# Performance work log

Measured on AMD Instinct MI355X. Metric: run time of the kernel, lower is better.

## Reference

```python
import jax, jax.numpy as jnp
import numpy as np

B, S, H, DH = 2, 2048, 24, 32
E = H * DH  # 768


def setup_inputs() -> dict:
    key = jax.random.key(0)
    ks = jax.random.split(key, 7)
    embedding = jax.random.normal(ks[0], (B, S, E), dtype=jnp.float32)
    mask = jax.random.randint(ks[1], (B, S, S), 0, 2).astype(bool)
    # per-head QKV weights (applied as x @ W, equivalent param to torch Linear W.T)
    Wq = jax.random.normal(ks[2], (H, DH, DH), dtype=jnp.float32) * 0.05
    Wk = jax.random.normal(ks[3], (H, DH, DH), dtype=jnp.float32) * 0.05
    Wv = jax.random.normal(ks[4], (H, DH, DH), dtype=jnp.float32) * 0.05
    Wo = jax.random.normal(ks[5], (E, E), dtype=jnp.float32) * 0.02
    bo = jax.random.normal(ks[6], (E,), dtype=jnp.float32) * 0.02
    return {"embedding": embedding, "mask": mask, "Wq": Wq, "Wk": Wk,
            "Wv": Wv, "Wo": Wo, "bo": bo}


def reference(embedding, mask, Wq, Wk, Wv, Wo, bo):
    # split channels into heads: [B,S,H,DH]
    xh = embedding.reshape(B, S, H, DH)
    # per-head projections (batched over heads)
    Q = jnp.einsum('bshd,hde->bhse', xh, Wq)
    K = jnp.einsum('bshd,hde->bhse', xh, Wk)
    V = jnp.einsum('bshd,hde->bhse', xh, Wv)
    scale = 1.0 / jnp.sqrt(jnp.float32(DH))
    scores = jnp.einsum('bhqd,bhkd->bhqk', Q, K) * scale
    # faithful quirk: masked positions set to -1e-6 (not -inf)
    scores = jnp.where(mask[:, None, :, :], scores, jnp.float32(-1e-6))
    probs = jax.nn.softmax(scores, axis=-1)
    out = jnp.einsum('bhqk,bhkd->bqhd', probs, V)  # [B,S,H,DH]
    out = out.reshape(B, S, E)  # concat heads along feature dim
    return out @ Wo.T + bo
```

## Files before the change

### kernel.cpp

```cpp
#include <hip/hip_runtime.h>
#include <hip/hip_bf16.h>

#define B_  2
#define S_  2048
#define H_  24
#define DH_ 32
#define E_  768
#define SW_ (S_/32)

#define NB_MASK ((B_*S_*S_)/256)
#define NB_WO   ((E_*E_)/1024)
#define NB_WT   (H_)

typedef __attribute__((ext_vector_type(8))) short short8;
typedef __attribute__((ext_vector_type(4))) float f32x4;

static __device__ __forceinline__ float bf16tof(short s) {
    unsigned u = ((unsigned)(unsigned short)s) << 16;
    return __builtin_bit_cast(float, u);
}
static __device__ __forceinline__ short4 pack4(float a, float b, float c, float d) {
    union { __hip_bfloat162 h[2]; short4 s; } u;
    u.h[0] = __float22bfloat162_rn(make_float2(a, b));
    u.h[1] = __float22bfloat162_rn(make_float2(c, d));
    return u.s;
}
static __device__ __forceinline__ short8 pack8f(const float* a, const float* b) {
    union { __hip_bfloat162 h[4]; short8 s; } u;
    u.h[0] = __float22bfloat162_rn(make_float2(a[0], a[1]));
    u.h[1] = __float22bfloat162_rn(make_float2(a[2], a[3]));
    u.h[2] = __float22bfloat162_rn(make_float2(b[0], b[1]));
    u.h[3] = __float22bfloat162_rn(make_float2(b[2], b[3]));
    return u.s;
}
static __device__ __forceinline__ short8 pack8(float4 a, float4 b) {
    union { __hip_bfloat162 h[4]; short8 s; } u;
    u.h[0] = __float22bfloat162_rn(make_float2(a.x, a.y));
    u.h[1] = __float22bfloat162_rn(make_float2(a.z, a.w));
    u.h[2] = __float22bfloat162_rn(make_float2(b.x, b.y));
    u.h[3] = __float22bfloat162_rn(make_float2(b.z, b.w));
    return u.s;
}

#define QSCALE  0.25503487f
#define MEXP    0.99999899864f

__global__ __launch_bounds__(256) void prep_kernel(
    const int* __restrict__ mask, const float* __restrict__ Wo,
    const float* __restrict__ Wq, const float* __restrict__ Wk,
    const float* __restrict__ Wv,
    unsigned int* __restrict__ mbits, __hip_bfloat16* __restrict__ Wob,
    __hip_bfloat16* __restrict__ WTq, __hip_bfloat16* __restrict__ WTk,
    __hip_bfloat16* __restrict__ WTv)
{
    const int bx = blockIdx.x;
    if (bx < NB_MASK) {
        const int idx  = bx * 256 + threadIdx.x;
        const int lane = threadIdx.x & 63;
        const unsigned long long bal = __ballot(mask[idx] != 0);
        if (lane == 0) {
            uint2 w;
            w.x = (unsigned int)(bal & 0xffffffffull);
            w.y = (unsigned int)(bal >> 32);
            *reinterpret_cast<uint2*>(mbits + (idx >> 5)) = w;
        }
    } else if (bx < NB_MASK + NB_WO) {
        const int i = ((bx - NB_MASK) * 256 + threadIdx.x) * 4;
        const float4 w = *reinterpret_cast<const float4*>(Wo + i);
        *reinterpret_cast<short4*>(Wob + i) = pack4(w.x, w.y, w.z, w.w);
    } else {
        const int h = bx - NB_MASK - NB_WO;
        const int base = h * DH_ * DH_;
        for (int i = threadIdx.x; i < DH_ * DH_; i += 256) {
            const int d = i >> 5, e = i & 31;
            WTq[base + e * 32 + d] = __float2bfloat16(Wq[base + i]);
            WTk[base + e * 32 + d] = __float2bfloat16(Wk[base + i]);
            WTv[base + e * 32 + d] = __float2bfloat16(Wv[base + i]);
        }
    }
}

__global__ __launch_bounds__(256) void qkv_kernel(
    const float* __restrict__ x,
    const __hip_bfloat16* __restrict__ WTq,
    const __hip_bfloat16* __restrict__ WTk,
    const __hip_bfloat16* __restrict__ WTv,
    __hip_bfloat16* __restrict__ Qo,
    __hip_bfloat16* __restrict__ Ko,
    __hip_bfloat16* __restrict__ Vto)
{
    const int bh   = blockIdx.y;
    const int b    = bh / H_;
    const int h    = bh - b * H_;
    const int wave = threadIdx.x >> 6;
    const int lane = threadIdx.x & 63;
    const int col  = lane & 15;
    const int quad = lane >> 4;
    const int sw   = blockIdx.x * 64 + wave * 16;
    const int s    = sw + col;

    const float* xp = x + ((size_t)b * S_ + s) * E_ + h * DH_ + quad * 8;
    const float4 xa = *reinterpret_cast<const float4*>(xp);
    const float4 xb = *reinterpret_cast<const float4*>(xp + 4);
    const short8 xf = pack8(xa, xb);

    const int wofs = h * DH_ * DH_ + col * 32 + quad * 8;
    const short8 aQ0 = *reinterpret_cast<const short8*>(WTq + wofs);
    const short8 aQ1 = *reinterpret_cast<const short8*>(WTq + wofs + 16 * 32);
    const short8 aK0 = *reinterpret_cast<const short8*>(WTk + wofs);
    const short8 aK1 = *reinterpret_cast<const short8*>(WTk + wofs + 16 * 32);
    const short8 bV0 = *reinterpret_cast<const short8*>(WTv + wofs);
    const short8 bV1 = *reinterpret_cast<const short8*>(WTv + wofs + 16 * 32);

    const f32x4 z = {0.f, 0.f, 0.f, 0.f};
    const f32x4 qt0 = __builtin_amdgcn_mfma_f32_16x16x32_bf16(aQ0, xf, z, 0, 0, 0);
    const f32x4 qt1 = __builtin_amdgcn_mfma_f32_16x16x32_bf16(aQ1, xf, z, 0, 0, 0);
    const f32x4 kt0 = __builtin_amdgcn_mfma_f32_16x16x32_bf16(aK0, xf, z, 0, 0, 0);
    const f32x4 kt1 = __builtin_amdgcn_mfma_f32_16x16x32_bf16(aK1, xf, z, 0, 0, 0);
    const f32x4 vv0 = __builtin_amdgcn_mfma_f32_16x16x32_bf16(xf, bV0, z, 0, 0, 0);
    const f32x4 vv1 = __builtin_amdgcn_mfma_f32_16x16x32_bf16(xf, bV1, z, 0, 0, 0);

    __hip_bfloat16* qrow = Qo + ((size_t)bh * S_ + s) * DH_;
    *reinterpret_cast<short4*>(qrow + quad * 4) =
        pack4(qt0[0] * QSCALE, qt0[1] * QSCALE, qt0[2] * QSCALE, qt0[3] * QSCALE);
    *reinterpret_cast<short4*>(qrow + 16 + quad * 4) =
        pack4(qt1[0] * QSCALE, qt1[1] * QSCALE, qt1[2] * QSCALE, qt1[3] * QSCALE);

    const int t32  = s & 31;
    const int slot = (s & ~31) | (((t32 >> 2) & 1) << 4)
                   | (((t32 >> 3) << 2) | (t32 & 3));
    __hip_bfloat16* krow = Ko + ((size_t)bh * S_ + slot) * DH_;
    *reinterpret_cast<short4*>(krow + quad * 4)      = pack4(kt0[0], kt0[1], kt0[2], kt0[3]);
    *reinterpret_cast<short4*>(krow + 16 + quad * 4) = pack4(kt1[0], kt1[1], kt1[2], kt1[3]);

    const int sb = sw + quad * 4;
    *reinterpret_cast<short4*>(Vto + ((size_t)bh * DH_ + col) * S_ + sb) =
        pack4(vv0[0], vv0[1], vv0[2], vv0[3]);
    *reinterpret_cast<short4*>(Vto + ((size_t)bh * DH_ + 16 + col) * S_ + sb) =
        pack4(vv1[0], vv1[1], vv1[2], vv1[3]);
}

__global__ __launch_bounds__(256) void attn_kernel(
    const __hip_bfloat16* __restrict__ Q,
    const __hip_bfloat16* __restrict__ K,
    const __hip_bfloat16* __restrict__ Vt,
    const unsigned int* __restrict__ mbits,
    __hip_bfloat16* __restrict__ Opart,
    float* __restrict__ lpart,
    int parts)
{
    const int bid  = blockIdx.x;
    const int xcd  = bid & 7;
    const int t_   = bid >> 3;
    const int bh   = xcd * 6 + (t_ % 6);
    const int rest = t_ / 6;
    const int qblk = rest & 7;
    const int part = rest >> 3;

    const int b    = bh / H_;
    const int h    = bh - b * H_;
    const int niter = S_ / (64 * parts);
    const int kbeg  = part * (S_ / parts);
    const int wave = threadIdx.x >> 6;
    const int lane = threadIdx.x & 63;
    const int col  = lane & 15;
    const int quad = lane >> 4;
    const int q0   = qblk * 256 + wave * 64;

    const __hip_bfloat16* Qbh = Q  + (size_t)bh * S_ * DH_;
    const __hip_bfloat16* Kbh = K  + (size_t)bh * S_ * DH_;
    const __hip_bfloat16* Vbh = Vt + (size_t)bh * DH_ * S_;

    short8 qf[4];
#pragma unroll
    for (int t = 0; t < 4; ++t)
        qf[t] = *reinterpret_cast<const short8*>(
            Qbh + (size_t)(q0 + t * 16 + col) * DH_ + quad * 8);

    const __hip_bfloat16* Kp  = Kbh + (size_t)(kbeg + col) * DH_ + quad * 8;
    const __hip_bfloat16* Vp0 = Vbh + (size_t)col * S_ + kbeg + quad * 8;
    const __hip_bfloat16* Vp1 = Vbh + (size_t)(16 + col) * S_ + kbeg + quad * 8;
    const unsigned int* mbb = mbits + (size_t)b * S_ * SW_ + (kbeg >> 5);
    const unsigned int* mp[4];
#pragma unroll
    for (int t = 0; t < 4; ++t)
        mp[t] = mbb + (size_t)(q0 + t * 16 + col) * SW_;

    const short ONE = 0x3F80;
    const short8 ones = {ONE, ONE, ONE, ONE, ONE, ONE, ONE, ONE};

    f32x4 o0a[4], o1a[4], la[4];
#pragma unroll
    for (int t = 0; t < 4; ++t) {
        o0a[t] = (f32x4){0.f,0.f,0.f,0.f};
        o1a[t] = (f32x4){0.f,0.f,0.f,0.f};
        la[t]  = (f32x4){0.f,0.f,0.f,0.f};
    }

    for (int it = 0; it < niter; ++it) {
        uint2 mw[4];
#pragma unroll
        for (int t = 0; t < 4; ++t)
            mw[t] = *reinterpret_cast<const uint2*>(mp[t]);

        const short8 kA0 = *reinterpret_cast<const short8*>(Kp);
        const short8 kA1 = *reinterpret_cast<const short8*>(Kp + 16 * DH_);
        const short8 vA0 = *reinterpret_cast<const short8*>(Vp0);
        const short8 vA1 = *reinterpret_cast<const short8*>(Vp1);
        const short8 kB0 = *reinterpret_cast<const short8*>(Kp + 32 * DH_);
        const short8 kB1 = *reinterpret_cast<const short8*>(Kp + 48 * DH_);
        const short8 vB0 = *reinterpret_cast<const short8*>(Vp0 + 32);
        const short8 vB1 = *reinterpret_cast<const short8*>(Vp1 + 32);

        const f32x4 z = {0.f, 0.f, 0.f, 0.f};

        f32x4 s0[4], s1[4];
#pragma unroll
        for (int t = 0; t < 4; ++t) {
            s0[t] = __builtin_amdgcn_mfma_f32_16x16x32_bf16(kA0, qf[t], z, 0, 0, 0);
            s1[t] = __builtin_amdgcn_mfma_f32_16x16x32_bf16(kA1, qf[t], z, 0, 0, 0);
        }
#pragma unroll
        for (int t = 0; t < 4; ++t) {
            float p0[4], p1[4];
#pragma unroll
            for (int r = 0; r < 4; ++r) {
                const int kb = quad * 8 + r;
                const float e0 = __builtin_amdgcn_exp2f(s0[t][r]);
                const float e1 = __builtin_amdgcn_exp2f(s1[t][r]);
                p0[r] = ((mw[t].x >> kb)       & 1u) ? e0 : MEXP;
                p1[r] = ((mw[t].x >> (kb + 4)) & 1u) ? e1 : MEXP;
            }
            const short8 pf = pack8f(p0, p1);
            o0a[t] = __builtin_amdgcn_mfma_f32_16x16x32_bf16(vA0, pf, o0a[t], 0, 0, 0);
            o1a[t] = __builtin_amdgcn_mfma_f32_16x16x32_bf16(vA1, pf, o1a[t], 0, 0, 0);
            la[t]  = __builtin_amdgcn_mfma_f32_16x16x32_bf16(ones, pf, la[t], 0, 0, 0);
        }

#pragma unroll
        for (int t = 0; t < 4; ++t) {
            s0[t] = __builtin_amdgcn_mfma_f32_16x16x32_bf16(kB0, qf[t], z, 0, 0, 0);
            s1[t] = __builtin_amdgcn_mfma_f32_16x16x32_bf16(kB1, qf[t], z, 0, 0, 0);
        }
#pragma unroll
        for (int t = 0; t < 4; ++t) {
            float p0[4], p1[4];
#pragma unroll
            for (int r = 0; r < 4; ++r) {
                const int kb = quad * 8 + r;
                const float e0 = __builtin_amdgcn_exp2f(s0[t][r]);
                const float e1 = __builtin_amdgcn_exp2f(s1[t][r]);
                p0[r] = ((mw[t].y >> kb)       & 1u) ? e0 : MEXP;
                p1[r] = ((mw[t].y >> (kb + 4)) & 1u) ? e1 : MEXP;
            }
            const short8 pf = pack8f(p0, p1);
            o0a[t] = __builtin_amdgcn_mfma_f32_16x16x32_bf16(vB0, pf, o0a[t], 0, 0, 0);
            o1a[t] = __builtin_amdgcn_mfma_f32_16x16x32_bf16(vB1, pf, o1a[t], 0, 0, 0);
            la[t]  = __builtin_amdgcn_mfma_f32_16x16x32_bf16(ones, pf, la[t], 0, 0, 0);
        }

        Kp  += 64 * DH_;
        Vp0 += 64;
        Vp1 += 64;
#pragma unroll
        for (int t = 0; t < 4; ++t) mp[t] += 2;
    }

    __hip_bfloat16* Ob = Opart + (size_t)part * B_ * S_ * E_;
    float* lp = lpart + (size_t)part * B_ * H_ * S_ + (size_t)bh * S_;
#pragma unroll
    for (int t = 0; t < 4; ++t) {
        __hip_bfloat16* orow = Ob + ((size_t)b * S_ + q0 + t * 16 + col) * E_ + h * DH_;
        *reinterpret_cast<short4*>(orow + quad * 4) =
            pack4(o0a[t][0], o0a[t][1], o0a[t][2], o0a[t][3]);
        *reinterpret_cast<short4*>(orow + 16 + quad * 4) =
            pack4(o1a[t][0], o1a[t][1], o1a[t][2], o1a[t][3]);
        if (quad == 0) lp[q0 + t * 16 + col] = la[t][0];
    }
}

template <int PARTS>
__global__ __launch_bounds__(256) void proj_kernel(
    const __hip_bfloat16* __restrict__ Opart,
    const float* __restrict__ lpart,
    const __hip_bfloat16* __restrict__ Wob,
    const float* __restrict__ bo,
    float* __restrict__ out)
{
    const int wave = threadIdx.x >> 6;
    const int lane = threadIdx.x & 63;
    const int col  = lane & 15;
    const int quad = lane >> 4;
    const int m0   = blockIdx.x * 16;
    const int n0   = blockIdx.y * 256 + wave * 64;

    const int m = m0 + col;
    const int b = m / S_;
    const int s = m - b * S_;
    const float* lpb = lpart + (size_t)(b * H_) * S_ + s;

    f32x4 acc[4] = {{0.f,0.f,0.f,0.f},{0.f,0.f,0.f,0.f},
                    {0.f,0.f,0.f,0.f},{0.f,0.f,0.f,0.f}};
    for (int k0 = 0; k0 < E_; k0 += 32) {
        const int h = k0 >> 5;
        const size_t aofs = (size_t)m * E_ + k0 + quad * 8;
        float av[8] = {0.f,0.f,0.f,0.f,0.f,0.f,0.f,0.f};
        float l = 0.f;
#pragma unroll
        for (int pp = 0; pp < PARTS; ++pp) {
            const short8 a = *reinterpret_cast<const short8*>(
                Opart + (size_t)pp * B_ * S_ * E_ + aofs);
            l += lpb[(size_t)pp * B_ * H_ * S_ + (size_t)h * S_];
#pragma unroll
            for (int i = 0; i < 8; ++i) av[i] += bf16tof(a[i]);
        }
        const float linv = 1.0f / l;
#pragma unroll
        for (int i = 0; i < 8; ++i) av[i] *= linv;
        const short8 af = pack8f(av, av + 4);

#pragma unroll
        for (int j = 0; j < 4; ++j) {
            const short8 bf = *reinterpret_cast<const short8*>(
                Wob + (size_t)(n0 + j * 16 + col) * E_ + k0 + quad * 8);
            acc[j] = __builtin_amdgcn_mfma_f32_16x16x32_bf16(af, bf, acc[j], 0, 0, 0);
        }
    }
#pragma unroll
    for (int j = 0; j < 4; ++j) {
        const int n = n0 + j * 16 + col;
        const float bias = bo[n];
#pragma unroll
        for (int r = 0; r < 4; ++r) {
            const int mm = m0 + quad * 4 + r;
            out[(size_t)mm * E_ + n] = acc[j][r] + bias;
        }
    }
}

extern "C" void kernel_launch(void* const* d_in, const int* in_sizes, int n_in,
                              void* d_out, int out_size, void* d_ws, size_t ws_size,
                              hipStream_t stream)
{
    const float* emb = (const float*)d_in[0];
    const int*   msk = (const int*)d_in[1];
    const float* Wq  = (const float*)d_in[2];
    const float* Wk  = (const float*)d_in[3];
    const float* Wv  = (const float*)d_in[4];
    const float* Wo  = (const float*)d_in[5];
    const float* bo  = (const float*)d_in[6];
    float* out = (float*)d_out;

    const size_t nqkv = (size_t)B_ * H_ * S_ * DH_;
    char* p = (char*)d_ws;
    __hip_bfloat16* Q    = (__hip_bfloat16*)p;  p += nqkv * 2;
    __hip_bfloat16* Kp   = (__hip_bfloat16*)p;  p += nqkv * 2;
    __hip_bfloat16* Vt   = (__hip_bfloat16*)p;  p += nqkv * 2;
    unsigned int*  mbits = (unsigned int*)p;    p += (size_t)B_ * S_ * SW_ * 4;
    __hip_bfloat16* Wob  = (__hip_bfloat16*)p;  p += (size_t)E_ * E_ * 2;
    __hip_bfloat16* WTq  = (__hip_bfloat16*)p;  p += (size_t)H_ * DH_ * DH_ * 2;
    __hip_bfloat16* WTk  = (__hip_bfloat16*)p;  p += (size_t)H_ * DH_ * DH_ * 2;
    __hip_bfloat16* WTv  = (__hip_bfloat16*)p;  p += (size_t)H_ * DH_ * DH_ * 2;
    __hip_bfloat16* Op   = (__hip_bfloat16*)p;
    const size_t base = (size_t)(p - (char*)d_ws);

    int parts = 1;
    {
        const size_t need = base + (size_t)2 * nqkv * 2
                          + (size_t)2 * B_ * H_ * S_ * 4;
        if (ws_size >= need) parts = 2;
    }
    float* lpart = (float*)(Op + (size_t)parts * nqkv);

    prep_kernel<<<NB_MASK + NB_WO + NB_WT, 256, 0, stream>>>(
        msk, Wo, Wq, Wk, Wv, mbits, Wob, WTq, WTk, WTv);
    qkv_kernel <<<dim3(S_ / 64, B_ * H_), 256, 0, stream>>>(
        emb, WTq, WTk, WTv, Q, Kp, Vt);
    attn_kernel<<<384 * parts, 256, 0, stream>>>(
        Q, Kp, Vt, mbits, Op, lpart, parts);
    if (parts == 2)
        proj_kernel<2><<<dim3((B_ * S_) / 16, E_ / 256), 256, 0, stream>>>(
            Op, lpart, Wob, bo, out);
    else
        proj_kernel<1><<<dim3((B_ * S_) / 16, E_ / 256), 256, 0, stream>>>(
            Op, lpart, Wob, bo, out);
}
```

Baseline: 233.5 us.

## Fuse QKV projection into prep kernel and switch output path to fp16

Merges the prep and QKV kernels into one launch. Each QKV block now gathers and converts its per-head weight fragments straight from the fp32 weights, so the separate transposed bf16 weight buffers go away. The attention partial outputs and Wo are stored as fp16 and the projection uses packed fp16 adds with the f16 MFMA. Masked probabilities use precomputed bit masks and 1.0 instead of MEXP, a small change to the masked-score value. It saves one launch and some dependency stalls, at the cost of redundant strided weight loads per block and reduced fp16 range.

```diff
diff --git a/kernel.cpp b/kernel.cpp
--- a/kernel.cpp
+++ b/kernel.cpp
@@ -8,17 +8,21 @@
 #define E_  768
 #define SW_ (S_/32)
 
+#define NB_QKV  ((S_/64)*(B_*H_))
 #define NB_MASK ((B_*S_*S_)/256)
 #define NB_WO   ((E_*E_)/1024)
-#define NB_WT   (H_)
 
 typedef __attribute__((ext_vector_type(8))) short short8;
 typedef __attribute__((ext_vector_type(4))) float f32x4;
-
-static __device__ __forceinline__ float bf16tof(short s) {
-    unsigned u = ((unsigned)(unsigned short)s) << 16;
-    return __builtin_bit_cast(float, u);
-}
+typedef _Float16 half8  __attribute__((ext_vector_type(8)));
+typedef _Float16 half2v __attribute__((ext_vector_type(2)));
+typedef __fp16   fp16x2 __attribute__((ext_vector_type(2)));
+
+static __device__ __forceinline__ half2v cvt2h(float a, float b) {
+    fp16x2 t = __builtin_amdgcn_cvt_pkrtz(a, b);
+    return __builtin_bit_cast(half2v, t);
+}
+
 static __device__ __forceinline__ short4 pack4(float a, float b, float c, float d) {
     union { __hip_bfloat162 h[2]; short4 s; } u;
     u.h[0] = __float22bfloat162_rn(make_float2(a, b));
@@ -41,21 +45,79 @@
     u.h[3] = __float22bfloat162_rn(make_float2(b.z, b.w));
     return u.s;
 }
+static __device__ __forceinline__ short8 wfrag(const float* __restrict__ Wb,
+                                               int quad, int eo) {
+    float w[8];
+#pragma unroll
+    for (int j = 0; j < 8; ++j) w[j] = Wb[(quad * 8 + j) * 32 + eo];
+    return pack8f(w, w + 4);
+}
 
 #define QSCALE  0.25503487f
-#define MEXP    0.99999899864f
-
-__global__ __launch_bounds__(256) void prep_kernel(
-    const int* __restrict__ mask, const float* __restrict__ Wo,
+
+__global__ __launch_bounds__(256) void prep_qkv_kernel(
+    const float* __restrict__ x, const int* __restrict__ mask,
+    const float* __restrict__ Wo,
     const float* __restrict__ Wq, const float* __restrict__ Wk,
     const float* __restrict__ Wv,
-    unsigned int* __restrict__ mbits, __hip_bfloat16* __restrict__ Wob,
-    __hip_bfloat16* __restrict__ WTq, __hip_bfloat16* __restrict__ WTk,
-    __hip_bfloat16* __restrict__ WTv)
+    __hip_bfloat16* __restrict__ Qo,
+    __hip_bfloat16* __restrict__ Ko,
+    __hip_bfloat16* __restrict__ Vto,
+    unsigned int* __restrict__ mbits, _Float16* __restrict__ Wob)
 {
     const int bx = blockIdx.x;
-    if (bx < NB_MASK) {
-        const int idx  = bx * 256 + threadIdx.x;
+    if (bx < NB_QKV) {
+        const int bh   = bx >> 5;
+        const int b    = bh / H_;
+        const int h    = bh - b * H_;
+        const int wave = threadIdx.x >> 6;
+        const int lane = threadIdx.x & 63;
+        const int col  = lane & 15;
+        const int quad = lane >> 4;
+        const int sw   = (bx & 31) * 64 + wave * 16;
+        const int s    = sw + col;
+
+        const float* xp = x + ((size_t)b * S_ + s) * E_ + h * DH_ + quad * 8;
+        const float4 xa = *reinterpret_cast<const float4*>(xp);
+        const float4 xb = *reinterpret_cast<const float4*>(xp + 4);
+        const short8 xf = pack8(xa, xb);
+
+        const int wb = h * DH_ * DH_;
+        const short8 aQ0 = wfrag(Wq + wb, quad, col);
+        const short8 aQ1 = wfrag(Wq + wb, quad, col + 16);
+        const short8 aK0 = wfrag(Wk + wb, quad, col);
+        const short8 aK1 = wfrag(Wk + wb, quad, col + 16);
+        const short8 bV0 = wfrag(Wv + wb, quad, col);
+        const short8 bV1 = wfrag(Wv + wb, quad, col + 16);
+
+        const f32x4 z = {0.f, 0.f, 0.f, 0.f};
+        const f32x4 qt0 = __builtin_amdgcn_mfma_f32_16x16x32_bf16(aQ0, xf, z, 0, 0, 0);
+        const f32x4 qt1 = __builtin_amdgcn_mfma_f32_16x16x32_bf16(aQ1, xf, z, 0, 0, 0);
+        const f32x4 kt0 = __builtin_amdgcn_mfma_f32_16x16x32_bf16(aK0, xf, z, 0, 0, 0);
+        const f32x4 kt1 = __builtin_amdgcn_mfma_f32_16x16x32_bf16(aK1, xf, z, 0, 0, 0);
+        const f32x4 vv0 = __builtin_amdgcn_mfma_f32_16x16x32_bf16(xf, bV0, z, 0, 0, 0);
+        const f32x4 vv1 = __builtin_amdgcn_mfma_f32_16x16x32_bf16(xf, bV1, z, 0, 0, 0);
+
+        __hip_bfloat16* qrow = Qo + ((size_t)bh * S_ + s) * DH_;
+        *reinterpret_cast<short4*>(qrow + quad * 4) =
+            pack4(qt0[0] * QSCALE, qt0[1] * QSCALE, qt0[2] * QSCALE, qt0[3] * QSCALE);
+        *reinterpret_cast<short4*>(qrow + 16 + quad * 4) =
+            pack4(qt1[0] * QSCALE, qt1[1] * QSCALE, qt1[2] * QSCALE, qt1[3] * QSCALE);
+
+        const int t32  = s & 31;
+        const int slot = (s & ~31) | (((t32 >> 2) & 1) << 4)
+                       | (((t32 >> 3) << 2) | (t32 & 3));
+        __hip_bfloat16* krow = Ko + ((size_t)bh * S_ + slot) * DH_;
+        *reinterpret_cast<short4*>(krow + quad * 4)      = pack4(kt0[0], kt0[1], kt0[2], kt0[3]);
+        *reinterpret_cast<short4*>(krow + 16 + quad * 4) = pack4(kt1[0], kt1[1], kt1[2], kt1[3]);
+
+        const int sb = sw + quad * 4;
+        *reinterpret_cast<short4*>(Vto + ((size_t)bh * DH_ + col) * S_ + sb) =
+            pack4(vv0[0], vv0[1], vv0[2], vv0[3]);
+        *reinterpret_cast<short4*>(Vto + ((size_t)bh * DH_ + 16 + col) * S_ + sb) =
+            pack4(vv1[0], vv1[1], vv1[2], vv1[3]);
+    } else if (bx < NB_QKV + NB_MASK) {
+        const int idx  = (bx - NB_QKV) * 256 + threadIdx.x;
         const int lane = threadIdx.x & 63;
         const unsigned long long bal = __ballot(mask[idx] != 0);
         if (lane == 0) {
@@ -64,80 +126,14 @@
             w.y = (unsigned int)(bal >> 32);
             *reinterpret_cast<uint2*>(mbits + (idx >> 5)) = w;
         }
-    } else if (bx < NB_MASK + NB_WO) {
-        const int i = ((bx - NB_MASK) * 256 + threadIdx.x) * 4;
+    } else {
+        const int i = ((bx - NB_QKV - NB_MASK) * 256 + threadIdx.x) * 4;
         const float4 w = *reinterpret_cast<const float4*>(Wo + i);
-        *reinterpret_cast<short4*>(Wob + i) = pack4(w.x, w.y, w.z, w.w);
-    } else {
-        const int h = bx - NB_MASK - NB_WO;
-        const int base = h * DH_ * DH_;
-        for (int i = threadIdx.x; i < DH_ * DH_; i += 256) {
-            const int d = i >> 5, e = i & 31;
-            WTq[base + e * 32 + d] = __float2bfloat16(Wq[base + i]);
-            WTk[base + e * 32 + d] = __float2bfloat16(Wk[base + i]);
-            WTv[base + e * 32 + d] = __float2bfloat16(Wv[base + i]);
-        }
-    }
-}
-
-__global__ __launch_bounds__(256) void qkv_kernel(
-    const float* __restrict__ x,
-    const __hip_bfloat16* __restrict__ WTq,
-    const __hip_bfloat16* __restrict__ WTk,
-    const __hip_bfloat16* __restrict__ WTv,
-    __hip_bfloat16* __restrict__ Qo,
-    __hip_bfloat16* __restrict__ Ko,
-    __hip_bfloat16* __restrict__ Vto)
-{
-    const int bh   = blockIdx.y;
-    const int b    = bh / H_;
-    const int h    = bh - b * H_;
-    const int wave = threadIdx.x >> 6;
-    const int lane = threadIdx.x & 63;
-    const int col  = lane & 15;
-    const int quad = lane >> 4;
-    const int sw   = blockIdx.x * 64 + wave * 16;
-    const int s    = sw + col;
-
-    const float* xp = x + ((size_t)b * S_ + s) * E_ + h * DH_ + quad * 8;
-    const float4 xa = *reinterpret_cast<const float4*>(xp);
-    const float4 xb = *reinterpret_cast<const float4*>(xp + 4);
-    const short8 xf = pack8(xa, xb);
-
-    const int wofs = h * DH_ * DH_ + col * 32 + quad * 8;
-    const short8 aQ0 = *reinterpret_cast<const short8*>(WTq + wofs);
-    const short8 aQ1 = *reinterpret_cast<const short8*>(WTq + wofs + 16 * 32);
-    const short8 aK0 = *reinterpret_cast<const short8*>(WTk + wofs);
-    const short8 aK1 = *reinterpret_cast<const short8*>(WTk + wofs + 16 * 32);
-    const short8 bV0 = *reinterpret_cast<const short8*>(WTv + wofs);
-    const short8 bV1 = *reinterpret_cast<const short8*>(WTv + wofs + 16 * 32);
-
-    const f32x4 z = {0.f, 0.f, 0.f, 0.f};
-    const f32x4 qt0 = __builtin_amdgcn_mfma_f32_16x16x32_bf16(aQ0, xf, z, 0, 0, 0);
-    const f32x4 qt1 = __builtin_amdgcn_mfma_f32_16x16x32_bf16(aQ1, xf, z, 0, 0, 0);
-    const f32x4 kt0 = __builtin_amdgcn_mfma_f32_16x16x32_bf16(aK0, xf, z, 0, 0, 0);
-    const f32x4 kt1 = __builtin_amdgcn_mfma_f32_16x16x32_bf16(aK1, xf, z, 0, 0, 0);
-    const f32x4 vv0 = __builtin_amdgcn_mfma_f32_16x16x32_bf16(xf, bV0, z, 0, 0, 0);
-    const f32x4 vv1 = __builtin_amdgcn_mfma_f32_16x16x32_bf16(xf, bV1, z, 0, 0, 0);
-
-    __hip_bfloat16* qrow = Qo + ((size_t)bh * S_ + s) * DH_;
-    *reinterpret_cast<short4*>(qrow + quad * 4) =
-        pack4(qt0[0] * QSCALE, qt0[1] * QSCALE, qt0[2] * QSCALE, qt0[3] * QSCALE);
-    *reinterpret_cast<short4*>(qrow + 16 + quad * 4) =
-        pack4(qt1[0] * QSCALE, qt1[1] * QSCALE, qt1[2] * QSCALE, qt1[3] * QSCALE);
-
-    const int t32  = s & 31;
-    const int slot = (s & ~31) | (((t32 >> 2) & 1) << 4)
-                   | (((t32 >> 3) << 2) | (t32 & 3));
-    __hip_bfloat16* krow = Ko + ((size_t)bh * S_ + slot) * DH_;
-    *reinterpret_cast<short4*>(krow + quad * 4)      = pack4(kt0[0], kt0[1], kt0[2], kt0[3]);
-    *reinterpret_cast<short4*>(krow + 16 + quad * 4) = pack4(kt1[0], kt1[1], kt1[2], kt1[3]);
-
-    const int sb = sw + quad * 4;
-    *reinterpret_cast<short4*>(Vto + ((size_t)bh * DH_ + col) * S_ + sb) =
-        pack4(vv0[0], vv0[1], vv0[2], vv0[3]);
-    *reinterpret_cast<short4*>(Vto + ((size_t)bh * DH_ + 16 + col) * S_ + sb) =
-        pack4(vv1[0], vv1[1], vv1[2], vv1[3]);
+        union { half2v h[2]; uint2 u; } uu;
+        uu.h[0] = cvt2h(w.x, w.y);
+        uu.h[1] = cvt2h(w.z, w.w);
+        *reinterpret_cast<uint2*>(Wob + i) = uu.u;
+    }
 }
 
 __global__ __launch_bounds__(256) void attn_kernel(
@@ -145,7 +141,7 @@
     const __hip_bfloat16* __restrict__ K,
     const __hip_bfloat16* __restrict__ Vt,
     const unsigned int* __restrict__ mbits,
-    __hip_bfloat16* __restrict__ Opart,
+    _Float16* __restrict__ Opart,
     float* __restrict__ lpart,
     int parts)
 {
@@ -186,6 +182,13 @@
     for (int t = 0; t < 4; ++t)
         mp[t] = mbb + (size_t)(q0 + t * 16 + col) * SW_;
 
+    unsigned bitL[4], bitH[4];
+#pragma unroll
+    for (int r = 0; r < 4; ++r) {
+        bitL[r] = 1u << (quad * 8 + r);
+        bitH[r] = 1u << (quad * 8 + 4 + r);
+    }
+
     const short ONE = 0x3F80;
     const short8 ones = {ONE, ONE, ONE, ONE, ONE, ONE, ONE, ONE};
 
@@ -225,11 +228,10 @@
             float p0[4], p1[4];
 #pragma unroll
             for (int r = 0; r < 4; ++r) {
-                const int kb = quad * 8 + r;
                 const float e0 = __builtin_amdgcn_exp2f(s0[t][r]);
                 const float e1 = __builtin_amdgcn_exp2f(s1[t][r]);
-                p0[r] = ((mw[t].x >> kb)       & 1u) ? e0 : MEXP;
-                p1[r] = ((mw[t].x >> (kb + 4)) & 1u) ? e1 : MEXP;
+                p0[r] = (mw[t].x & bitL[r]) ? e0 : 1.0f;
+                p1[r] = (mw[t].x & bitH[r]) ? e1 : 1.0f;
             }
             const short8 pf = pack8f(p0, p1);
             o0a[t] = __builtin_amdgcn_mfma_f32_16x16x32_bf16(vA0, pf, o0a[t], 0, 0, 0);
@@ -247,11 +249,10 @@
             float p0[4], p1[4];
 #pragma unroll
             for (int r = 0; r < 4; ++r) {
-                const int kb = quad * 8 + r;
                 const float e0 = __builtin_amdgcn_exp2f(s0[t][r]);
                 const float e1 = __builtin_amdgcn_exp2f(s1[t][r]);
-                p0[r] = ((mw[t].y >> kb)       & 1u) ? e0 : MEXP;
-                p1[r] = ((mw[t].y >> (kb + 4)) & 1u) ? e1 : MEXP;
+                p0[r] = (mw[t].y & bitL[r]) ? e0 : 1.0f;
+                p1[r] = (mw[t].y & bitH[r]) ? e1 : 1.0f;
             }
             const short8 pf = pack8f(p0, p1);
             o0a[t] = __builtin_amdgcn_mfma_f32_16x16x32_bf16(vB0, pf, o0a[t], 0, 0, 0);
@@ -266,24 +267,27 @@
         for (int t = 0; t < 4; ++t) mp[t] += 2;
     }
 
-    __hip_bfloat16* Ob = Opart + (size_t)part * B_ * S_ * E_;
+    _Float16* Ob = Opart + (size_t)part * B_ * S_ * E_;
     float* lp = lpart + (size_t)part * B_ * H_ * S_ + (size_t)bh * S_;
 #pragma unroll
     for (int t = 0; t < 4; ++t) {
-        __hip_bfloat16* orow = Ob + ((size_t)b * S_ + q0 + t * 16 + col) * E_ + h * DH_;
-        *reinterpret_cast<short4*>(orow + quad * 4) =
-            pack4(o0a[t][0], o0a[t][1], o0a[t][2], o0a[t][3]);
-        *reinterpret_cast<short4*>(orow + 16 + quad * 4) =
-            pack4(o1a[t][0], o1a[t][1], o1a[t][2], o1a[t][3]);
+        union { half2v h[2]; uint2 u; } u0, u1;
+        u0.h[0] = cvt2h(o0a[t][0], o0a[t][1]);
+        u0.h[1] = cvt2h(o0a[t][2], o0a[t][3]);
+        u1.h[0] = cvt2h(o1a[t][0], o1a[t][1]);
+        u1.h[1] = cvt2h(o1a[t][2], o1a[t][3]);
+        _Float16* orow = Ob + ((size_t)b * S_ + q0 + t * 16 + col) * E_ + h * DH_;
+        *reinterpret_cast<uint2*>(orow + quad * 4)      = u0.u;
+        *reinterpret_cast<uint2*>(orow + 16 + quad * 4) = u1.u;
         if (quad == 0) lp[q0 + t * 16 + col] = la[t][0];
     }
 }
 
 template <int PARTS>
 __global__ __launch_bounds__(256) void proj_kernel(
-    const __hip_bfloat16* __restrict__ Opart,
+    const _Float16* __restrict__ Opart,
     const float* __restrict__ lpart,
-    const __hip_bfloat16* __restrict__ Wob,
+    const _Float16* __restrict__ Wob,
     const float* __restrict__ bo,
     float* __restrict__ out)
 {
@@ -304,26 +308,31 @@
     for (int k0 = 0; k0 < E_; k0 += 32) {
         const int h = k0 >> 5;
         const size_t aofs = (size_t)m * E_ + k0 + quad * 8;
-        float av[8] = {0.f,0.f,0.f,0.f,0.f,0.f,0.f,0.f};
-        float l = 0.f;
-#pragma unroll
-        for (int pp = 0; pp < PARTS; ++pp) {
-            const short8 a = *reinterpret_cast<const short8*>(
-                Opart + (size_t)pp * B_ * S_ * E_ + aofs);
-            l += lpb[(size_t)pp * B_ * H_ * S_ + (size_t)h * S_];
-#pragma unroll
-            for (int i = 0; i < 8; ++i) av[i] += bf16tof(a[i]);
-        }
-        const float linv = 1.0f / l;
-#pragma unroll
-        for (int i = 0; i < 8; ++i) av[i] *= linv;
-        const short8 af = pack8f(av, av + 4);
+
+        float l = lpb[(size_t)h * S_];
+        if (PARTS == 2) l += lpb[(size_t)B_ * H_ * S_ + (size_t)h * S_];
+        const float linv = __builtin_amdgcn_rcpf(l);
+        const half2v lv = cvt2h(linv, linv);
+
+        union UA { uint4 u; half2v h[4]; half8 v; } ua;
+        ua.u = *reinterpret_cast<const uint4*>(Opart + aofs);
+        if (PARTS == 2) {
+            union UA ub;
+            ub.u = *reinterpret_cast<const uint4*>(
+                Opart + (size_t)B_ * S_ * E_ + aofs);
+#pragma unroll
+            for (int i = 0; i < 4; ++i) ua.h[i] += ub.h[i];
+        }
+#pragma unroll
+        for (int i = 0; i < 4; ++i) ua.h[i] *= lv;
+        const half8 af = ua.v;
 
 #pragma unroll
         for (int j = 0; j < 4; ++j) {
-            const short8 bf = *reinterpret_cast<const short8*>(
+            union UA wb;
+            wb.u = *reinterpret_cast<const uint4*>(
                 Wob + (size_t)(n0 + j * 16 + col) * E_ + k0 + quad * 8);
-            acc[j] = __builtin_amdgcn_mfma_f32_16x16x32_bf16(af, bf, acc[j], 0, 0, 0);
+            acc[j] = __builtin_amdgcn_mfma_f32_16x16x32_f16(af, wb.v, acc[j], 0, 0, 0);
         }
     }
 #pragma unroll
@@ -357,11 +366,8 @@
     __hip_bfloat16* Kp   = (__hip_bfloat16*)p;  p += nqkv * 2;
     __hip_bfloat16* Vt   = (__hip_bfloat16*)p;  p += nqkv * 2;
     unsigned int*  mbits = (unsigned int*)p;    p += (size_t)B_ * S_ * SW_ * 4;
-    __hip_bfloat16* Wob  = (__hip_bfloat16*)p;  p += (size_t)E_ * E_ * 2;
-    __hip_bfloat16* WTq  = (__hip_bfloat16*)p;  p += (size_t)H_ * DH_ * DH_ * 2;
-    __hip_bfloat16* WTk  = (__hip_bfloat16*)p;  p += (size_t)H_ * DH_ * DH_ * 2;
-    __hip_bfloat16* WTv  = (__hip_bfloat16*)p;  p += (size_t)H_ * DH_ * DH_ * 2;
-    __hip_bfloat16* Op   = (__hip_bfloat16*)p;
+    _Float16*      Wob   = (_Float16*)p;        p += (size_t)E_ * E_ * 2;
+    _Float16*      Op    = (_Float16*)p;
     const size_t base = (size_t)(p - (char*)d_ws);
 
     int parts = 1;
@@ -372,10 +378,8 @@
     }
     float* lpart = (float*)(Op + (size_t)parts * nqkv);
 
-    prep_kernel<<<NB_MASK + NB_WO + NB_WT, 256, 0, stream>>>(
-        msk, Wo, Wq, Wk, Wv, mbits, Wob, WTq, WTk, WTv);
-    qkv_kernel <<<dim3(S_ / 64, B_ * H_), 256, 0, stream>>>(
-        emb, WTq, WTk, WTv, Q, Kp, Vt);
+    prep_qkv_kernel<<<NB_QKV + NB_MASK + NB_WO, 256, 0, stream>>>(
+        emb, msk, Wo, Wq, Wk, Wv, Q, Kp, Vt, mbits, Wob);
     attn_kernel<<<384 * parts, 256, 0, stream>>>(
         Q, Kp, Vt, mbits, Op, lpart, parts);
     if (parts == 2)
```

New measurement: 233.8 us. Within noise of the previous version (+0.1%).
